# Optimization experiments

Measured on AMD Instinct MI355X. Metric: run time of the kernel, lower is better.

The kernel has to match this reference:

```python
import jax, jax.numpy as jnp
import numpy as np

FACTOR = 3
N_HEADS = 8


def prob_attention(q, k, v, key):
    # q,k,v: [B, L, H, D]  (Informer ProbAttention, mask_flag falsy, scale=None)
    B, L_Q, H, D = q.shape
    L_K = k.shape[1]
    Q = jnp.swapaxes(q, 1, 2)  # [B,H,L_Q,D]
    K = jnp.swapaxes(k, 1, 2)
    V = jnp.swapaxes(v, 1, 2)
    U_part = min(FACTOR * int(np.ceil(np.log(L_K))), L_K)  # sampled keys per query
    u = min(FACTOR * int(np.ceil(np.log(L_Q))), L_Q)       # active (top) queries
    idx = jax.random.randint(key, (L_Q, U_part), 0, L_K)   # shared across B,H like torch.randint
    K_sample = K[:, :, idx, :]                              # [B,H,L_Q,U_part,D] gather
    QK_sample = jnp.einsum('bhld,bhlsd->bhls', Q, K_sample)
    M = QK_sample.max(axis=-1) - QK_sample.sum(axis=-1) / L_K  # sparsity measure
    _, top_idx = jax.lax.top_k(M, u)                        # [B,H,u]
    Q_reduce = jnp.take_along_axis(Q, top_idx[..., None], axis=2)  # [B,H,u,D]
    scale = 1.0 / np.sqrt(D)
    scores = jnp.einsum('bhud,bhkd->bhuk', Q_reduce, K) * scale     # [B,H,u,L_K]
    attn = jax.nn.softmax(scores, axis=-1)
    out_top = jnp.einsum('bhuk,bhkd->bhud', attn, V)
    # initial context: mean of V over keys, broadcast to every query position
    context = jnp.broadcast_to(V.mean(axis=2, keepdims=True), (B, H, L_Q, D))
    bi = jnp.arange(B)[:, None, None]
    hi = jnp.arange(H)[None, :, None]
    context = context.at[bi, hi, top_idx].set(out_top)
    return jnp.swapaxes(context, 1, 2)  # [B,L_Q,H,D]


def attention_layer(xq, xk, xv, wq, bq, wk, bk, wv, bv, wo, bo, key):
    B, Lq, dm = xq.shape
    Lk = xk.shape[1]
    dk = dm // N_HEADS
    q = (xq @ wq + bq).reshape(B, Lq, N_HEADS, dk)
    k = (xk @ wk + bk).reshape(B, Lk, N_HEADS, dk)
    v = (xv @ wv + bv).reshape(B, Lk, N_HEADS, dk)
    out = prob_attention(q, k, v, key).reshape(B, Lq, dm)
    return out @ wo + bo


def setup_inputs() -> dict:
    key = jax.random.key(0)
    ks = jax.random.split(key, 20)
    B, Ld, Lp, dm = 4, 4096, 4096, 512
    inp = {
        'xs': jax.random.normal(ks[0], (B, Ld + Lp, dm), jnp.float32),
        'xd': jax.random.normal(ks[1], (B, Ld, dm), jnp.float32),
        'xp': jax.random.normal(ks[2], (B, Lp, dm), jnp.float32),
    }
    names = ['w0q', 'w0k', 'w0v', 'w0o', 'b0q', 'b0k', 'b0v', 'b0o',
             'w1q', 'w1k', 'w1v', 'w1o', 'b1q', 'b1k', 'b1v', 'b1o']
    for i, n in enumerate(names):
        if n.startswith('w'):
            inp[n] = jax.random.normal(ks[3 + i], (dm, dm), jnp.float32) * 0.02
        else:
            inp[n] = jnp.zeros((dm,), jnp.float32)
    return inp


def reference(xs, xd, xp,
              w0q, w0k, w0v, w0o, b0q, b0k, b0v, b0o,
              w1q, w1k, w1v, w1o, b1q, b1k, b1v, b1o):
    # dropout layers are identity in eval mode
    xp2 = attention_layer(xp, xd, xd, w0q, b0q, w0k, b0k, w0v, b0v, w0o, b0o,
                          jax.random.key(42))
    xd2 = attention_layer(xd, xp2, xp2, w1q, b1q, w1k, b1k, w1v, b1v, w1o, b1o,
                          jax.random.key(43))
    return xs + jnp.concatenate([xd2, xp2], axis=1)
```

## Files before the change

kernel.cpp:

```cpp
#include <hip/hip_runtime.h>
#include <math.h>

#define NB 4
#define SEQ 4096
#define DM 512
#define NH 8
#define HD 64
#define UU 27
#define NIDX (SEQ*UU)
#define NC 32
#define CS 128
#define PSTRIDE 66
#define LDP 40

typedef unsigned int u32;
typedef __attribute__((ext_vector_type(8))) short short8;
typedef __attribute__((ext_vector_type(4))) float f32x4;

__host__ __device__ inline u32 rotl32(u32 x, u32 r){ return (x<<r)|(x>>(32u-r)); }

__host__ __device__ inline void threefry2x32(u32 k0, u32 k1, u32 x0, u32 x1, u32* o0, u32* o1)
{
  u32 ks[3] = { k0, k1, k0 ^ k1 ^ 0x1BD11BDAu };
  x0 += ks[0]; x1 += ks[1];
  const u32 rotA[4] = {13u,15u,26u,6u};
  const u32 rotB[4] = {17u,29u,16u,24u};
  for (int i = 0; i < 5; i++) {
    const u32* rot = (i & 1) ? rotB : rotA;
    for (int j = 0; j < 4; j++) { x0 += x1; x1 = rotl32(x1, rot[j]); x1 ^= x0; }
    x0 += ks[(i+1)%3];
    x1 += ks[(i+2)%3] + (u32)(i+1);
  }
  *o0 = x0; *o1 = x1;
}

__global__ __launch_bounds__(256) void gen_idx_kernel(u32 k2a, u32 k2b, int* __restrict__ idx)
{
  int i = blockIdx.x * 256 + threadIdx.x;
  if (i >= NIDX) return;
  u32 o0, o1;
  threefry2x32(k2a, k2b, 0u, (u32)i, &o0, &o1);
  idx[i] = (int)((o0 ^ o1) & (SEQ - 1));
}

__device__ inline unsigned short f2bf_rne(float f) {
  u32 u = __float_as_uint(f);
  return (unsigned short)((u + 0x7fffu + ((u >> 16) & 1u)) >> 16);
}
__device__ inline void f2bf_split(float f, unsigned short& hi, unsigned short& lo) {
  u32 u = __float_as_uint(f);
  unsigned short h = (unsigned short)(u >> 16);
  float hf = __uint_as_float(((u32)h) << 16);
  hi = h;
  lo = f2bf_rne(f - hf);
}

template<int SPLIT>
__global__ __launch_bounds__(256) void gemm_mfma(
    const float* __restrict__ A, const float* __restrict__ W,
    const float* __restrict__ bias, float* __restrict__ C,
    const float* __restrict__ resid, int rowJump)
{
  __shared__ short As_hi[128 * LDP];
  __shared__ short Ws_hi[128 * LDP];
  __shared__ short As_lo[SPLIT ? 128 * LDP : 8];
  __shared__ short Ws_lo[SPLIT ? 128 * LDP : 8];

  const int t  = threadIdx.x;
  const int rb = blockIdx.x * 128;
  const int cb = blockIdx.y * 128;

  const int sa_row = t >> 1, sa_kh = (t & 1) * 16;
  const float* Ap = A + (long)(rb + sa_row) * DM + sa_kh;
  const int sw_n = t & 127, sw_kb = t >> 7;
  const float* Wp = W + cb + sw_n;

  const int lane = t & 63, wv = t >> 6;
  const int wm = (wv & 1) * 64, wn = (wv >> 1) * 64;
  const int fr = lane & 15, fq = lane >> 4;

  f32x4 acc[4][4];
  #pragma unroll
  for (int i = 0; i < 4; i++)
    #pragma unroll
    for (int j = 0; j < 4; j++) acc[i][j] = (f32x4)(0.f);

  for (int k0 = 0; k0 < DM; k0 += 32) {
    float a_f[16];
    *(float4*)&a_f[0]  = *(const float4*)(Ap + k0);
    *(float4*)&a_f[4]  = *(const float4*)(Ap + k0 + 4);
    *(float4*)&a_f[8]  = *(const float4*)(Ap + k0 + 8);
    *(float4*)&a_f[12] = *(const float4*)(Ap + k0 + 12);
    float w_f[16];
    #pragma unroll
    for (int j = 0; j < 8; j++) w_f[j]     = Wp[(long)(k0 + sw_kb * 8 + j) * DM];
    #pragma unroll
    for (int j = 0; j < 8; j++) w_f[8 + j] = Wp[(long)(k0 + (sw_kb + 2) * 8 + j) * DM];

    __syncthreads();

    union { short8 v[2]; unsigned short s[16]; } ah, al, wh, wl;
    if (SPLIT) {
      #pragma unroll
      for (int e = 0; e < 16; e++) f2bf_split(a_f[e], ah.s[e], al.s[e]);
      #pragma unroll
      for (int e = 0; e < 16; e++) f2bf_split(w_f[e], wh.s[e], wl.s[e]);
    } else {
      #pragma unroll
      for (int e = 0; e < 16; e++) ah.s[e] = f2bf_rne(a_f[e]);
      #pragma unroll
      for (int e = 0; e < 16; e++) wh.s[e] = f2bf_rne(w_f[e]);
    }
    *(short8*)&As_hi[sa_row * LDP + sa_kh]     = ah.v[0];
    *(short8*)&As_hi[sa_row * LDP + sa_kh + 8] = ah.v[1];
    *(short8*)&Ws_hi[sw_n * LDP + sw_kb * 8]        = wh.v[0];
    *(short8*)&Ws_hi[sw_n * LDP + (sw_kb + 2) * 8]  = wh.v[1];
    if (SPLIT) {
      *(short8*)&As_lo[sa_row * LDP + sa_kh]     = al.v[0];
      *(short8*)&As_lo[sa_row * LDP + sa_kh + 8] = al.v[1];
      *(short8*)&Ws_lo[sw_n * LDP + sw_kb * 8]        = wl.v[0];
      *(short8*)&Ws_lo[sw_n * LDP + (sw_kb + 2) * 8]  = wl.v[1];
    }
    __syncthreads();

    short8 a_hi[4], b_hi[4];
    #pragma unroll
    for (int i = 0; i < 4; i++)
      a_hi[i] = *(const short8*)&As_hi[(wm + i * 16 + fr) * LDP + fq * 8];
    #pragma unroll
    for (int j = 0; j < 4; j++)
      b_hi[j] = *(const short8*)&Ws_hi[(wn + j * 16 + fr) * LDP + fq * 8];
    #pragma unroll
    for (int i = 0; i < 4; i++)
      #pragma unroll
      for (int j = 0; j < 4; j++)
        acc[i][j] = __builtin_amdgcn_mfma_f32_16x16x32_bf16(a_hi[i], b_hi[j], acc[i][j], 0, 0, 0);
    if (SPLIT) {
      short8 a_lo[4], b_lo[4];
      #pragma unroll
      for (int i = 0; i < 4; i++)
        a_lo[i] = *(const short8*)&As_lo[(wm + i * 16 + fr) * LDP + fq * 8];
      #pragma unroll
      for (int j = 0; j < 4; j++)
        b_lo[j] = *(const short8*)&Ws_lo[(wn + j * 16 + fr) * LDP + fq * 8];
      #pragma unroll
      for (int i = 0; i < 4; i++)
        #pragma unroll
        for (int j = 0; j < 4; j++) {
          acc[i][j] = __builtin_amdgcn_mfma_f32_16x16x32_bf16(a_hi[i], b_lo[j], acc[i][j], 0, 0, 0);
          acc[i][j] = __builtin_amdgcn_mfma_f32_16x16x32_bf16(a_lo[i], b_hi[j], acc[i][j], 0, 0, 0);
        }
    }
  }

  #pragma unroll
  for (int j = 0; j < 4; j++) {
    int col = cb + wn + j * 16 + fr;
    float bv = bias[col];
    #pragma unroll
    for (int i = 0; i < 4; i++) {
      int row0 = rb + wm + i * 16 + fq * 4;
      #pragma unroll
      for (int r = 0; r < 4; r++) {
        int row = row0 + r;
        long off = (long)row * DM + (long)(row >> 12) * rowJump + col;
        float v = acc[i][j][r] + bv;
        if (resid) v += resid[off];
        C[off] = v;
      }
    }
  }
}

__global__ __launch_bounds__(256) void mscore_kernel(const float* __restrict__ Q, const float* __restrict__ K,
                                                     const int* __restrict__ idx, float* __restrict__ M)
{
  const int wl = threadIdx.x >> 6, lane = threadIdx.x & 63;
  const int bl = blockIdx.x * 4 + wl;
  const int b = bl >> 12, l = bl & (SEQ - 1);

  const float4* qp = (const float4*)(Q + (long)bl * DM + lane * 8);
  float4 q0 = qp[0], q1 = qp[1];

  const int* ip = idx + l * UU;
  int idxv = ip[lane < UU ? lane : 0];
  int chv = idxv >> 9;

  const float* kb = K + ((long)b << 12) * DM + lane * 8;
  float mx = -INFINITY, sm = 0.f;
  #pragma unroll 1
  for (int c = 0; c < 8; c++) {
    unsigned long long msk = __ballot(chv == c) & ((1ull << UU) - 1ull);
    while (msk) {
      int s = __builtin_ctzll(msk);
      msk &= msk - 1;
      int kl = __shfl(idxv, s, 64);
      const float4* kp = (const float4*)(kb + (long)kl * DM);
      float4 k0 = kp[0], k1 = kp[1];
      float dot;
      dot = q0.x * k0.x;
      dot = fmaf(q0.y, k0.y, dot); dot = fmaf(q0.z, k0.z, dot); dot = fmaf(q0.w, k0.w, dot);
      dot = fmaf(q1.x, k1.x, dot); dot = fmaf(q1.y, k1.y, dot);
      dot = fmaf(q1.z, k1.z, dot); dot = fmaf(q1.w, k1.w, dot);
      dot += __shfl_xor(dot, 1, 64);
      dot += __shfl_xor(dot, 2, 64);
      dot += __shfl_xor(dot, 4, 64);
      mx = fmaxf(mx, dot);
      sm += dot;
    }
  }
  if ((lane & 7) == 0) {
    int h = lane >> 3;
    M[(((long)b * NH + h) << 12) + l] = mx - sm * (1.0f / (float)SEQ);
  }
}

__global__ __launch_bounds__(256) void topk_kernel(const float* __restrict__ M, int* __restrict__ topidx)
{
  __shared__ float vals[SEQ];
  __shared__ float rv[256];
  __shared__ int   ri[256];
  const float* m = M + (long)blockIdx.x * SEQ;
  for (int i = threadIdx.x; i < SEQ; i += 256) vals[i] = m[i];
  __syncthreads();
  for (int it = 0; it < UU; it++) {
    float bv = -INFINITY; int bi = 0x7fffffff;
    for (int i = threadIdx.x; i < SEQ; i += 256) {
      float v = vals[i];
      if (v > bv) { bv = v; bi = i; }
    }
    rv[threadIdx.x] = bv; ri[threadIdx.x] = bi;
    __syncthreads();
    for (int s = 128; s > 0; s >>= 1) {
      if (threadIdx.x < s) {
        float ov = rv[threadIdx.x + s]; int oi = ri[threadIdx.x + s];
        if (ov > rv[threadIdx.x] || (ov == rv[threadIdx.x] && oi < ri[threadIdx.x])) {
          rv[threadIdx.x] = ov; ri[threadIdx.x] = oi;
        }
      }
      __syncthreads();
    }
    if (threadIdx.x == 0) { topidx[blockIdx.x * UU + it] = ri[0]; vals[ri[0]] = -INFINITY; }
    __syncthreads();
  }
}

__global__ __launch_bounds__(512) void vmean_partial(const float* __restrict__ V, float* __restrict__ vsum)
{
  int b = blockIdx.x >> 5, chunk = blockIdx.x & 31;
  int c = threadIdx.x;
  const float* p = V + ((long)b * SEQ + chunk * 128) * DM + c;
  float s = 0.f;
  for (int l = 0; l < 128; l++) s += p[(long)l * DM];
  atomicAdd(&vsum[b * DM + c], s);
}

__global__ __launch_bounds__(256) void attn_part(const float* __restrict__ Q, const float* __restrict__ K,
                                                 const float* __restrict__ V, const int* __restrict__ topidx,
                                                 float* __restrict__ partial)
{
  __shared__ float Qs[UU][HD];
  __shared__ float S[UU][CS];
  __shared__ float Vt[CS][HD];
  __shared__ float m_s[UU], l_s[UU];

  const int t = threadIdx.x;
  const int bh = blockIdx.x;
  const int chunk = blockIdx.y;
  const int b = bh >> 3, h = bh & 7;
  const long kbase = ((long)(b << 12) + chunk * CS) * DM + h * HD;
  const int* tp = topidx + bh * UU;

  for (int i = t; i < UU * HD; i += 256) {
    int u = i >> 6, d = i & 63;
    Qs[u][d] = Q[((long)(b << 12) + tp[u]) * DM + h * HD + d];
  }
  for (int i = t; i < CS * (HD / 4); i += 256) {
    int row = i >> 4, c4 = (i & 15) << 2;
    *(float4*)&Vt[row][c4] = *(const float4*)(V + kbase + (long)row * DM + c4);
  }
  __syncthreads();

  {
    const int l = t >> 1, half = t & 1, d0 = half * 32;
    const float* kp = K + kbase + (long)l * DM + d0;
    float4 kr[8];
    #pragma unroll
    for (int j = 0; j < 8; j++) kr[j] = *(const float4*)(kp + j * 4);
    #pragma unroll 1
    for (int u = 0; u < UU; u++) {
      const float4* qf = (const float4*)&Qs[u][d0];
      float dot = 0.f;
      #pragma unroll
      for (int j = 0; j < 8; j++) {
        float4 q = qf[j];
        dot = fmaf(q.x, kr[j].x, dot); dot = fmaf(q.y, kr[j].y, dot);
        dot = fmaf(q.z, kr[j].z, dot); dot = fmaf(q.w, kr[j].w, dot);
      }
      float tot = dot + __shfl_xor(dot, 1, 64);
      if (half == 0) S[u][l] = tot * 0.125f;
    }
  }
  __syncthreads();

  {
    const int u = t >> 3, il = t & 7;
    if (u < UU) {
      float mx = -INFINITY;
      for (int l = il; l < CS; l += 8) mx = fmaxf(mx, S[u][l]);
      #pragma unroll
      for (int m = 1; m < 8; m <<= 1) mx = fmaxf(mx, __shfl_xor(mx, m, 64));
      float ps = 0.f;
      for (int l = il; l < CS; l += 8) {
        float e = expf(S[u][l] - mx);
        S[u][l] = e;
        ps += e;
      }
      #pragma unroll
      for (int m = 1; m < 8; m <<= 1) ps += __shfl_xor(ps, m, 64);
      if (il == 0) { m_s[u] = mx; l_s[u] = ps; }
    }
  }
  __syncthreads();

  {
    const int d = t & 63, g = t >> 6;
    for (int u = g; u < UU; u += 4) {
      float acc = 0.f;
      #pragma unroll 4
      for (int l = 0; l < CS; l += 4) {
        float4 p4 = *(const float4*)&S[u][l];
        acc = fmaf(p4.x, Vt[l][d],     acc);
        acc = fmaf(p4.y, Vt[l + 1][d], acc);
        acc = fmaf(p4.z, Vt[l + 2][d], acc);
        acc = fmaf(p4.w, Vt[l + 3][d], acc);
      }
      float* pp = partial + (((long)bh * NC + chunk) * UU + u) * PSTRIDE;
      pp[2 + d] = acc;
      if (d == 0) { pp[0] = m_s[u]; pp[1] = l_s[u]; }
    }
  }
}

__global__ __launch_bounds__(64) void attn_merge(const float* __restrict__ partial, const int* __restrict__ topidx,
                                                 float* __restrict__ ctx)
{
  int g = blockIdx.x;
  int bh = g / UU, u = g % UU;
  int b = bh >> 3, h = bh & 7;
  int d = threadIdx.x;
  float M = -INFINITY, S = 0.f, acc = 0.f;
  for (int c = 0; c < NC; c++) {
    const float* pp = partial + (((long)bh * NC + c) * UU + u) * PSTRIDE;
    float mc = pp[0], sc = pp[1], a = pp[2 + d];
    if (mc > M) {
      float r = expf(M - mc);
      acc *= r; S *= r; M = mc;
    }
    float w = expf(mc - M);
    acc = fmaf(a, w, acc);
    S = fmaf(sc, w, S);
  }
  int ql = topidx[g];
  ctx[((long)(b << 12) + ql) * DM + h * HD + d] = acc / S;
}

__global__ __launch_bounds__(256) void ctx_fill(const float* __restrict__ vsum, float* __restrict__ ctx)
{
  long g = (long)blockIdx.x * 256 + threadIdx.x;
  int b = (int)(g >> 19);
  int c4 = (int)(g & 127);
  float4 v = ((const float4*)vsum)[b * 128 + c4];
  const float s = 1.0f / (float)SEQ;
  v.x *= s; v.y *= s; v.z *= s; v.w *= s;
  ((float4*)ctx)[g] = v;
}

__global__ __launch_bounds__(256) void add_upper(const float* __restrict__ xs, const float* __restrict__ xp2,
                                                 float* __restrict__ out)
{
  long g = (long)blockIdx.x * 256 + threadIdx.x;
  int b = (int)(g >> 19);
  long rem = g & 524287;
  float4 p = ((const float4*)xp2)[g];
  long o = ((long)b * 8192 + SEQ) * 128 + rem;
  float4 x = ((const float4*)xs)[o];
  x.x += p.x; x.y += p.y; x.z += p.z; x.w += p.w;
  ((float4*)out)[o] = x;
}

extern "C" void kernel_launch(void* const* d_in, const int* in_sizes, int n_in,
                              void* d_out, int out_size, void* d_ws, size_t ws_size,
                              hipStream_t stream)
{
  const float* xs  = (const float*)d_in[0];
  const float* xd  = (const float*)d_in[1];
  const float* xp  = (const float*)d_in[2];
  const float* w0q = (const float*)d_in[3];
  const float* w0k = (const float*)d_in[4];
  const float* w0v = (const float*)d_in[5];
  const float* w0o = (const float*)d_in[6];
  const float* b0q = (const float*)d_in[7];
  const float* b0k = (const float*)d_in[8];
  const float* b0v = (const float*)d_in[9];
  const float* b0o = (const float*)d_in[10];
  const float* w1q = (const float*)d_in[11];
  const float* w1k = (const float*)d_in[12];
  const float* w1v = (const float*)d_in[13];
  const float* w1o = (const float*)d_in[14];
  const float* b1q = (const float*)d_in[15];
  const float* b1k = (const float*)d_in[16];
  const float* b1v = (const float*)d_in[17];
  const float* b1o = (const float*)d_in[18];
  float* out = (float*)d_out;

  const long BIG = (long)NB * SEQ * DM;
  float* A  = (float*)d_ws;
  float* Bb = A  + BIG;
  float* Cc = Bb + BIG;
  float* Dd = Cc + BIG;
  float* ex = Dd + BIG;
  int*   idxbuf = (int*)ex;
  float* Mbuf   = ex + NIDX;
  int*   topidx = (int*)(Mbuf + (long)NB * NH * SEQ);
  float* vsum   = (float*)(topidx + NB * NH * UU);

  dim3 gg(128, 4);
  dim3 ag(NB * NH, NC);
  u32 k2a, k2b;

  threefry2x32(0u, 42u, 0u, 1u, &k2a, &k2b);
  gen_idx_kernel<<<(NIDX + 255) / 256, 256, 0, stream>>>(k2a, k2b, idxbuf);
  gemm_mfma<1><<<gg, 256, 0, stream>>>(xp, w0q, b0q, A,  nullptr, 0);
  gemm_mfma<1><<<gg, 256, 0, stream>>>(xd, w0k, b0k, Bb, nullptr, 0);
  gemm_mfma<1><<<gg, 256, 0, stream>>>(xd, w0v, b0v, Cc, nullptr, 0);
  mscore_kernel<<<NB * SEQ / 4, 256, 0, stream>>>(A, Bb, idxbuf, Mbuf);
  topk_kernel<<<NB * NH, 256, 0, stream>>>(Mbuf, topidx);
  hipMemsetAsync(vsum, 0, NB * DM * sizeof(float), stream);
  vmean_partial<<<NB * 32, 512, 0, stream>>>(Cc, vsum);
  attn_part<<<ag, 256, 0, stream>>>(A, Bb, Cc, topidx, Dd);
  ctx_fill<<<8192, 256, 0, stream>>>(vsum, A);
  attn_merge<<<NB * NH * UU, 64, 0, stream>>>(Dd, topidx, A);
  gemm_mfma<1><<<gg, 256, 0, stream>>>(A, w0o, b0o, Bb, nullptr, 0);
  add_upper<<<8192, 256, 0, stream>>>(xs, Bb, out);

  threefry2x32(0u, 43u, 0u, 1u, &k2a, &k2b);
  gen_idx_kernel<<<(NIDX + 255) / 256, 256, 0, stream>>>(k2a, k2b, idxbuf);
  gemm_mfma<1><<<gg, 256, 0, stream>>>(xd, w1q, b1q, A,  nullptr, 0);
  gemm_mfma<1><<<gg, 256, 0, stream>>>(Bb, w1k, b1k, Cc, nullptr, 0);
  gemm_mfma<0><<<gg, 256, 0, stream>>>(Bb, w1v, b1v, Dd, nullptr, 0);
  mscore_kernel<<<NB * SEQ / 4, 256, 0, stream>>>(A, Cc, idxbuf, Mbuf);
  topk_kernel<<<NB * NH, 256, 0, stream>>>(Mbuf, topidx);
  hipMemsetAsync(vsum, 0, NB * DM * sizeof(float), stream);
  vmean_partial<<<NB * 32, 512, 0, stream>>>(Dd, vsum);
  attn_part<<<ag, 256, 0, stream>>>(A, Cc, Dd, topidx, Bb);
  ctx_fill<<<8192, 256, 0, stream>>>(vsum, A);
  attn_merge<<<NB * NH * UU, 64, 0, stream>>>(Bb, topidx, A);
  gemm_mfma<0><<<gg, 256, 0, stream>>>(A, w1o, b1o, out, xs, SEQ * DM);
}
```

Before: 849.3 us.

## Pre-split activations and weights to bf16 hi/lo once, feed GEMMs bf16

Adds kernels that convert fp32 activations and all eight weight matrices into separate bf16 hi/lo planes, with weights stored transposed. The GEMMs then load bf16 directly with contiguous 16-byte loads instead of converting per tile and doing strided weight reads. The attention merge and context fill write bf16 hi/lo directly, and the xd conversion is shared by three GEMMs. In exchange it adds extra memory traffic and launches for the conversion passes, and the two GEMMs that used single bf16 now use the split path with more MFMA work.

```diff
diff --git a/kernel.cpp b/kernel.cpp
--- a/kernel.cpp
+++ b/kernel.cpp
@@ -14,7 +14,9 @@
 #define LDP 40
 
 typedef unsigned int u32;
+typedef unsigned short u16;
 typedef __attribute__((ext_vector_type(8))) short short8;
+typedef __attribute__((ext_vector_type(4))) short short4v;
 typedef __attribute__((ext_vector_type(4))) float f32x4;
 
 __host__ __device__ inline u32 rotl32(u32 x, u32 r){ return (x<<r)|(x>>(32u-r)); }
@@ -43,21 +45,51 @@
   idx[i] = (int)((o0 ^ o1) & (SEQ - 1));
 }
 
-__device__ inline unsigned short f2bf_rne(float f) {
+__device__ inline u16 f2bf_rne(float f) {
   u32 u = __float_as_uint(f);
-  return (unsigned short)((u + 0x7fffu + ((u >> 16) & 1u)) >> 16);
-}
-__device__ inline void f2bf_split(float f, unsigned short& hi, unsigned short& lo) {
+  return (u16)((u + 0x7fffu + ((u >> 16) & 1u)) >> 16);
+}
+__device__ inline void f2bf_split(float f, u16& hi, u16& lo) {
   u32 u = __float_as_uint(f);
-  unsigned short h = (unsigned short)(u >> 16);
+  u16 h = (u16)(u >> 16);
   float hf = __uint_as_float(((u32)h) << 16);
   hi = h;
   lo = f2bf_rne(f - hf);
 }
 
+__global__ __launch_bounds__(256) void conv_split(const float* __restrict__ X,
+                                                  u16* __restrict__ hi, u16* __restrict__ lo)
+{
+  long g = (long)blockIdx.x * 256 + threadIdx.x;
+  float4 x0 = ((const float4*)X)[g * 2];
+  float4 x1 = ((const float4*)X)[g * 2 + 1];
+  union { short8 v; u16 s[8]; } h, l;
+  float xv[8] = { x0.x, x0.y, x0.z, x0.w, x1.x, x1.y, x1.z, x1.w };
+  #pragma unroll
+  for (int e = 0; e < 8; e++) f2bf_split(xv[e], h.s[e], l.s[e]);
+  ((short8*)hi)[g] = h.v;
+  ((short8*)lo)[g]  = l.v;
+}
+
+struct WPtrs { const float* w[8]; };
+__global__ __launch_bounds__(256) void convw_kernel(WPtrs wp, u16* __restrict__ outp)
+{
+  const int n  = blockIdx.x;
+  const int wi = blockIdx.y;
+  const float* W = wp.w[wi];
+  u16* hi = outp + (long)wi * 524288 + n * DM;
+  u16* lo = hi + 262144;
+  for (int k = threadIdx.x; k < DM; k += 256) {
+    u16 h, l;
+    f2bf_split(W[(long)k * DM + n], h, l);
+    hi[k] = h; lo[k] = l;
+  }
+}
+
 template<int SPLIT>
-__global__ __launch_bounds__(256) void gemm_mfma(
-    const float* __restrict__ A, const float* __restrict__ W,
+__global__ __launch_bounds__(256) void gemm_bf(
+    const u16* __restrict__ Ah, const u16* __restrict__ Al,
+    const u16* __restrict__ Wh, const u16* __restrict__ Wl,
     const float* __restrict__ bias, float* __restrict__ C,
     const float* __restrict__ resid, int rowJump)
 {
@@ -70,10 +102,24 @@
   const int rb = blockIdx.x * 128;
   const int cb = blockIdx.y * 128;
 
-  const int sa_row = t >> 1, sa_kh = (t & 1) * 16;
-  const float* Ap = A + (long)(rb + sa_row) * DM + sa_kh;
-  const int sw_n = t & 127, sw_kb = t >> 7;
-  const float* Wp = W + cb + sw_n;
+  const int r0 = t >> 2, sg = (t & 3) * 8;
+  const u16* pAh0 = Ah + (long)(rb + r0) * DM + sg;
+  const u16* pAh1 = pAh0 + (long)64 * DM;
+  const u16* pWh0 = Wh + (long)(cb + r0) * DM + sg;
+  const u16* pWh1 = pWh0 + (long)64 * DM;
+  const u16* pAl0 = SPLIT ? (Al + (long)(rb + r0) * DM + sg) : pAh0;
+  const u16* pAl1 = pAl0 + (long)64 * DM;
+  const u16* pWl0 = SPLIT ? (Wl + (long)(cb + r0) * DM + sg) : pWh0;
+  const u16* pWl1 = pWl0 + (long)64 * DM;
+
+  short* dA0 = &As_hi[r0 * LDP + sg];
+  short* dA1 = &As_hi[(r0 + 64) * LDP + sg];
+  short* dW0 = &Ws_hi[r0 * LDP + sg];
+  short* dW1 = &Ws_hi[(r0 + 64) * LDP + sg];
+  short* dAl0 = &As_lo[SPLIT ? r0 * LDP + sg : 0];
+  short* dAl1 = &As_lo[SPLIT ? (r0 + 64) * LDP + sg : 0];
+  short* dWl0 = &Ws_lo[SPLIT ? r0 * LDP + sg : 0];
+  short* dWl1 = &Ws_lo[SPLIT ? (r0 + 64) * LDP + sg : 0];
 
   const int lane = t & 63, wv = t >> 6;
   const int wm = (wv & 1) * 64, wn = (wv >> 1) * 64;
@@ -86,40 +132,25 @@
     for (int j = 0; j < 4; j++) acc[i][j] = (f32x4)(0.f);
 
   for (int k0 = 0; k0 < DM; k0 += 32) {
-    float a_f[16];
-    *(float4*)&a_f[0]  = *(const float4*)(Ap + k0);
-    *(float4*)&a_f[4]  = *(const float4*)(Ap + k0 + 4);
-    *(float4*)&a_f[8]  = *(const float4*)(Ap + k0 + 8);
-    *(float4*)&a_f[12] = *(const float4*)(Ap + k0 + 12);
-    float w_f[16];
-    #pragma unroll
-    for (int j = 0; j < 8; j++) w_f[j]     = Wp[(long)(k0 + sw_kb * 8 + j) * DM];
-    #pragma unroll
-    for (int j = 0; j < 8; j++) w_f[8 + j] = Wp[(long)(k0 + (sw_kb + 2) * 8 + j) * DM];
+    short8 va0 = *(const short8*)(pAh0 + k0);
+    short8 va1 = *(const short8*)(pAh1 + k0);
+    short8 vw0 = *(const short8*)(pWh0 + k0);
+    short8 vw1 = *(const short8*)(pWh1 + k0);
+    short8 la0, la1, lw0, lw1;
+    if (SPLIT) {
+      la0 = *(const short8*)(pAl0 + k0);
+      la1 = *(const short8*)(pAl1 + k0);
+      lw0 = *(const short8*)(pWl0 + k0);
+      lw1 = *(const short8*)(pWl1 + k0);
+    }
 
     __syncthreads();
 
-    union { short8 v[2]; unsigned short s[16]; } ah, al, wh, wl;
+    *(short8*)dA0 = va0; *(short8*)dA1 = va1;
+    *(short8*)dW0 = vw0; *(short8*)dW1 = vw1;
     if (SPLIT) {
-      #pragma unroll
-      for (int e = 0; e < 16; e++) f2bf_split(a_f[e], ah.s[e], al.s[e]);
-      #pragma unroll
-      for (int e = 0; e < 16; e++) f2bf_split(w_f[e], wh.s[e], wl.s[e]);
-    } else {
-      #pragma unroll
-      for (int e = 0; e < 16; e++) ah.s[e] = f2bf_rne(a_f[e]);
-      #pragma unroll
-      for (int e = 0; e < 16; e++) wh.s[e] = f2bf_rne(w_f[e]);
-    }
-    *(short8*)&As_hi[sa_row * LDP + sa_kh]     = ah.v[0];
-    *(short8*)&As_hi[sa_row * LDP + sa_kh + 8] = ah.v[1];
-    *(short8*)&Ws_hi[sw_n * LDP + sw_kb * 8]        = wh.v[0];
-    *(short8*)&Ws_hi[sw_n * LDP + (sw_kb + 2) * 8]  = wh.v[1];
-    if (SPLIT) {
-      *(short8*)&As_lo[sa_row * LDP + sa_kh]     = al.v[0];
-      *(short8*)&As_lo[sa_row * LDP + sa_kh + 8] = al.v[1];
-      *(short8*)&Ws_lo[sw_n * LDP + sw_kb * 8]        = wl.v[0];
-      *(short8*)&Ws_lo[sw_n * LDP + (sw_kb + 2) * 8]  = wl.v[1];
+      *(short8*)dAl0 = la0; *(short8*)dAl1 = la1;
+      *(short8*)dWl0 = lw0; *(short8*)dWl1 = lw1;
     }
     __syncthreads();
 
@@ -342,8 +373,8 @@
   }
 }
 
-__global__ __launch_bounds__(64) void attn_merge(const float* __restrict__ partial, const int* __restrict__ topidx,
-                                                 float* __restrict__ ctx)
+__global__ __launch_bounds__(64) void attn_merge_bf(const float* __restrict__ partial, const int* __restrict__ topidx,
+                                                    u16* __restrict__ hi, u16* __restrict__ lo)
 {
   int g = blockIdx.x;
   int bh = g / UU, u = g % UU;
@@ -362,18 +393,26 @@
     S = fmaf(sc, w, S);
   }
   int ql = topidx[g];
-  ctx[((long)(b << 12) + ql) * DM + h * HD + d] = acc / S;
-}
-
-__global__ __launch_bounds__(256) void ctx_fill(const float* __restrict__ vsum, float* __restrict__ ctx)
+  long o = ((long)(b << 12) + ql) * DM + h * HD + d;
+  u16 hv, lv;
+  f2bf_split(acc / S, hv, lv);
+  hi[o] = hv; lo[o] = lv;
+}
+
+__global__ __launch_bounds__(256) void ctx_fill_bf(const float* __restrict__ vsum,
+                                                   u16* __restrict__ hi, u16* __restrict__ lo)
 {
   long g = (long)blockIdx.x * 256 + threadIdx.x;
   int b = (int)(g >> 19);
   int c4 = (int)(g & 127);
   float4 v = ((const float4*)vsum)[b * 128 + c4];
   const float s = 1.0f / (float)SEQ;
-  v.x *= s; v.y *= s; v.z *= s; v.w *= s;
-  ((float4*)ctx)[g] = v;
+  float xv[4] = { v.x * s, v.y * s, v.z * s, v.w * s };
+  union { short4v v; u16 s[4]; } h, l;
+  #pragma unroll
+  for (int e = 0; e < 4; e++) f2bf_split(xv[e], h.s[e], l.s[e]);
+  ((short4v*)hi)[g] = h.v;
+  ((short4v*)lo)[g]  = l.v;
 }
 
 __global__ __launch_bounds__(256) void add_upper(const float* __restrict__ xs, const float* __restrict__ xp2,
@@ -420,41 +459,58 @@
   float* Cc = Bb + BIG;
   float* Dd = Cc + BIG;
   float* ex = Dd + BIG;
+  float* Pq  = ex + BIG;
+  float* Pkv = Pq + BIG;
+
   int*   idxbuf = (int*)ex;
   float* Mbuf   = ex + NIDX;
   int*   topidx = (int*)(Mbuf + (long)NB * NH * SEQ);
   float* vsum   = (float*)(topidx + NB * NH * UU);
+  u16*   wpl    = (u16*)(ex + (1 << 20));
+
+  u16* Pq_hi  = (u16*)Pq;   u16* Pq_lo  = Pq_hi  + BIG;
+  u16* Pkv_hi = (u16*)Pkv;  u16* Pkv_lo = Pkv_hi + BIG;
+  auto whi = [&](int i){ return wpl + (long)i * 524288; };
+  auto wlo = [&](int i){ return wpl + (long)i * 524288 + 262144; };
 
   dim3 gg(128, 4);
   dim3 ag(NB * NH, NC);
   u32 k2a, k2b;
 
+  WPtrs wp;
+  wp.w[0] = w0q; wp.w[1] = w0k; wp.w[2] = w0v; wp.w[3] = w0o;
+  wp.w[4] = w1q; wp.w[5] = w1k; wp.w[6] = w1v; wp.w[7] = w1o;
+  convw_kernel<<<dim3(512, 8), 256, 0, stream>>>(wp, wpl);
+
   threefry2x32(0u, 42u, 0u, 1u, &k2a, &k2b);
   gen_idx_kernel<<<(NIDX + 255) / 256, 256, 0, stream>>>(k2a, k2b, idxbuf);
-  gemm_mfma<1><<<gg, 256, 0, stream>>>(xp, w0q, b0q, A,  nullptr, 0);
-  gemm_mfma<1><<<gg, 256, 0, stream>>>(xd, w0k, b0k, Bb, nullptr, 0);
-  gemm_mfma<1><<<gg, 256, 0, stream>>>(xd, w0v, b0v, Cc, nullptr, 0);
+  conv_split<<<4096, 256, 0, stream>>>(xp, Pq_hi, Pq_lo);
+  conv_split<<<4096, 256, 0, stream>>>(xd, Pkv_hi, Pkv_lo);
+  gemm_bf<1><<<gg, 256, 0, stream>>>(Pq_hi,  Pq_lo,  whi(0), wlo(0), b0q, A,  nullptr, 0);
+  gemm_bf<1><<<gg, 256, 0, stream>>>(Pkv_hi, Pkv_lo, whi(1), wlo(1), b0k, Bb, nullptr, 0);
+  gemm_bf<1><<<gg, 256, 0, stream>>>(Pkv_hi, Pkv_lo, whi(2), wlo(2), b0v, Cc, nullptr, 0);
   mscore_kernel<<<NB * SEQ / 4, 256, 0, stream>>>(A, Bb, idxbuf, Mbuf);
   topk_kernel<<<NB * NH, 256, 0, stream>>>(Mbuf, topidx);
   hipMemsetAsync(vsum, 0, NB * DM * sizeof(float), stream);
   vmean_partial<<<NB * 32, 512, 0, stream>>>(Cc, vsum);
   attn_part<<<ag, 256, 0, stream>>>(A, Bb, Cc, topidx, Dd);
-  ctx_fill<<<8192, 256, 0, stream>>>(vsum, A);
-  attn_merge<<<NB * NH * UU, 64, 0, stream>>>(Dd, topidx, A);
-  gemm_mfma<1><<<gg, 256, 0, stream>>>(A, w0o, b0o, Bb, nullptr, 0);
+  ctx_fill_bf<<<8192, 256, 0, stream>>>(vsum, Pq_hi, Pq_lo);
+  attn_merge_bf<<<NB * NH * UU, 64, 0, stream>>>(Dd, topidx, Pq_hi, Pq_lo);
+  gemm_bf<1><<<gg, 256, 0, stream>>>(Pq_hi, Pq_lo, whi(3), wlo(3), b0o, Bb, nullptr, 0);
   add_upper<<<8192, 256, 0, stream>>>(xs, Bb, out);
 
   threefry2x32(0u, 43u, 0u, 1u, &k2a, &k2b);
   gen_idx_kernel<<<(NIDX + 255) / 256, 256, 0, stream>>>(k2a, k2b, idxbuf);
-  gemm_mfma<1><<<gg, 256, 0, stream>>>(xd, w1q, b1q, A,  nullptr, 0);
-  gemm_mfma<1><<<gg, 256, 0, stream>>>(Bb, w1k, b1k, Cc, nullptr, 0);
-  gemm_mfma<0><<<gg, 256, 0, stream>>>(Bb, w1v, b1v, Dd, nullptr, 0);
+  gemm_bf<1><<<gg, 256, 0, stream>>>(Pkv_hi, Pkv_lo, whi(4), wlo(4), b1q, A, nullptr, 0);
+  conv_split<<<4096, 256, 0, stream>>>(Bb, Pq_hi, Pq_lo);
+  gemm_bf<1><<<gg, 256, 0, stream>>>(Pq_hi, Pq_lo, whi(5), wlo(5), b1k, Cc, nullptr, 0);
+  gemm_bf<1><<<gg, 256, 0, stream>>>(Pq_hi, Pq_lo, whi(6), wlo(6), b1v, Dd, nullptr, 0);
   mscore_kernel<<<NB * SEQ / 4, 256, 0, stream>>>(A, Cc, idxbuf, Mbuf);
   topk_kernel<<<NB * NH, 256, 0, stream>>>(Mbuf, topidx);
   hipMemsetAsync(vsum, 0, NB * DM * sizeof(float), stream);
   vmean_partial<<<NB * 32, 512, 0, stream>>>(Dd, vsum);
   attn_part<<<ag, 256, 0, stream>>>(A, Cc, Dd, topidx, Bb);
-  ctx_fill<<<8192, 256, 0, stream>>>(vsum, A);
-  attn_merge<<<NB * NH * UU, 64, 0, stream>>>(Bb, topidx, A);
-  gemm_mfma<0><<<gg, 256, 0, stream>>>(A, w1o, b1o, out, xs, SEQ * DM);
-}
+  ctx_fill_bf<<<8192, 256, 0, stream>>>(vsum, Pkv_hi, Pkv_lo);
+  attn_merge_bf<<<NB * NH * UU, 64, 0, stream>>>(Bb, topidx, Pkv_hi, Pkv_lo);
+  gemm_bf<1><<<gg, 256, 0, stream>>>(Pkv_hi, Pkv_lo, whi(7), wlo(7), b1o, out, xs, SEQ * DM);
+}
```

Result: no change. 863.4 us (+1.7%).
